# Kernel optimization log

Measured on AMD Instinct MI355X. Metric: run time of the kernel, lower is better.

Reference implementation:

```python
import jax, jax.numpy as jnp
import numpy as np

DIM = 512
HEADS = 8
DIM_HEAD = 64
DIM_INNER = HEADS * DIM_HEAD
SCALE = DIM_HEAD ** -0.5


def setup_inputs() -> dict:
    key = jax.random.key(0)
    ks = jax.random.split(key, 8)
    b, n = 2, 1024
    x = jax.random.normal(ks[0], (b, n, DIM), dtype=jnp.float32)
    w = lambda k, i, o: jax.random.normal(k, (i, o), dtype=jnp.float32) * 0.02
    return {
        'x': x,
        'w_q_u': w(ks[1], DIM, DIM_INNER),
        'w_k_u': w(ks[2], DIM, DIM_INNER),
        'w_v_u': w(ks[3], DIM, DIM_INNER),
        'w_q_c': w(ks[4], DIM, DIM_INNER),
        'w_k_c': w(ks[5], DIM, DIM_INNER),
        'w_v_c': w(ks[6], DIM, DIM_INNER),
        'w_out': w(ks[7], DIM_INNER, DIM),
    }


def reference(x, w_q_u, w_k_u, w_v_u, w_q_c, w_k_c, w_v_c, w_out):
    b, n, _ = x.shape

    def proj(w):  # [b,n,dim] -> [b,h,n,d]
        return (x @ w).reshape(b, n, HEADS, DIM_HEAD).transpose(0, 2, 1, 3)

    q_u, k_u, v_u = proj(w_q_u), proj(w_k_u), proj(w_v_u)
    q_c, k_c, v_c = proj(w_q_c), proj(w_k_c), proj(w_v_c)

    idx = jnp.arange(n)
    causal = idx[:, None] >= idx[None, :]  # tril ones (binary causal mask)

    # term1 = (q_c @ v_u^T) * scale, zeroed above diagonal
    term1 = jnp.einsum('bhid,bhjd->bhij', q_c, v_u) * SCALE
    term1 = term1 * causal.astype(term1.dtype)

    # sigmoid term: (q_u @ k_u^T)*scale with lookahead mask tril(-inf, diag=0)
    logits_u = jnp.einsum('bhid,bhjd->bhij', q_u, k_u) * SCALE
    sig = jax.nn.sigmoid(jnp.where(causal, -jnp.inf, logits_u))

    # S_u[i,k] = sum_j term1[i,j] * sig[k,j]
    S_u = jnp.einsum('bhij,bhkj->bhik', term1, sig)

    # S_c: causal-masked QK
    S_c = jnp.einsum('bhid,bhjd->bhij', q_c, k_c) * SCALE
    S_c = jnp.where(causal, S_c, -jnp.inf)

    final_scores = S_c - jax.nn.silu(S_u)
    attn = jax.nn.softmax(final_scores, axis=-1)
    out = jnp.einsum('bhij,bhjd->bhid', attn, v_c)  # [b,h,n,d]
    out = out.transpose(0, 2, 1, 3).reshape(b, n, DIM_INNER)
    return out @ w_out
```

## Files before the change

### kernel.cpp

```cpp
#include <hip/hip_runtime.h>
#include <math.h>


typedef __bf16 bf16x8 __attribute__((ext_vector_type(8)));
typedef float f32x4 __attribute__((ext_vector_type(4)));

#define SCALE 0.125f

#define GLL(g, l) __builtin_amdgcn_global_load_lds(                         \
    (const __attribute__((address_space(1))) void*)(g),                     \
    (__attribute__((address_space(3))) void*)(l), 16, 0, 0)

__device__ __forceinline__ unsigned short f2bf(float f){
  unsigned int x = __builtin_bit_cast(unsigned int, f);
  unsigned int r = (x + 0x7fffu + ((x >> 16) & 1u)) >> 16;
  return (unsigned short)r;
}
__device__ __forceinline__ float bf2f(unsigned short u){
  unsigned int x = ((unsigned int)u) << 16;
  return __builtin_bit_cast(float, x);
}
__device__ __forceinline__ f32x4 mfma16(bf16x8 a, bf16x8 b, f32x4 c){
  return __builtin_amdgcn_mfma_f32_16x16x32_bf16(a, b, c, 0, 0, 0);
}
__device__ __forceinline__ bf16x8 ld8(const unsigned short* p){
  return *(const bf16x8*)p;
}

__global__ __launch_bounds__(256) void k_prep(
    const float* __restrict__ x,
    const float* __restrict__ w0, const float* __restrict__ w1,
    const float* __restrict__ w2, const float* __restrict__ w3,
    const float* __restrict__ w4, const float* __restrict__ w5,
    const float* __restrict__ w6,
    unsigned short* __restrict__ xb, unsigned short* __restrict__ wT){
  int t = threadIdx.x;
  if (blockIdx.x < 1024){
    int i = blockIdx.x * 256 + t;
    float4 v = ((const float4*)x)[i];
    ushort4 o; o.x = f2bf(v.x); o.y = f2bf(v.y); o.z = f2bf(v.z); o.w = f2bf(v.w);
    ((ushort4*)xb)[i] = o;
    return;
  }
  __shared__ float lds[64 * 65];
  int bx = blockIdx.x - 1024;
  int mat = bx >> 6, tile = bx & 63, tr = tile >> 3, tc = tile & 7;
  int k0 = tr * 64, c0 = tc * 64;
  const float* src;
  switch (mat){
    case 0: src = w0; break; case 1: src = w1; break; case 2: src = w2; break;
    case 3: src = w3; break; case 4: src = w4; break; case 5: src = w5; break;
    default: src = w6; break;
  }
#pragma unroll
  for (int i = 0; i < 4; ++i){
    int r = (t >> 4) + i * 16, c4 = (t & 15) * 4;
    float4 v = *(const float4*)(src + (size_t)(k0 + r) * 512 + c0 + c4);
    lds[r * 65 + c4 + 0] = v.x; lds[r * 65 + c4 + 1] = v.y;
    lds[r * 65 + c4 + 2] = v.z; lds[r * 65 + c4 + 3] = v.w;
  }
  __syncthreads();
  unsigned short* dst = wT + (size_t)mat * 262144;
#pragma unroll
  for (int i = 0; i < 4; ++i){
    int oc = (t >> 4) + i * 16;
    int kq = (t & 15) * 4;
    ushort4 o;
    o.x = f2bf(lds[(kq + 0) * 65 + oc]);
    o.y = f2bf(lds[(kq + 1) * 65 + oc]);
    o.z = f2bf(lds[(kq + 2) * 65 + oc]);
    o.w = f2bf(lds[(kq + 3) * 65 + oc]);
    *(ushort4*)(dst + (size_t)(c0 + oc) * 512 + k0 + kq) = o;
  }
}

__global__ __launch_bounds__(256) void k_proj(
    const unsigned short* __restrict__ xb, const unsigned short* __restrict__ wT,
    unsigned short* __restrict__ P){
  __shared__ unsigned short sA[128 * 32], sB[128 * 32];
  int t = threadIdx.x, lane = t & 63, l16 = lane & 15, quad = lane >> 4;
  int w = t >> 6, wm = w >> 1, wn = w & 1;
  int bx = blockIdx.x;
  int mt = bx / 24, nt = bx - mt * 24;
  int M0 = mt * 128, N0 = nt * 128;
  int matb = N0 >> 9;
  int nin = N0 & 511;
  int srow = (lane >> 2), scol = (lane & 3) * 8;
  const unsigned short* gA = xb + (size_t)(M0 + w*32 + srow) * 512 + scol;
  const unsigned short* gB = wT + (size_t)matb * 262144
                               + (size_t)(nin + w*32 + srow) * 512 + scol;
  unsigned short* lA = sA + (w*32) * 32;
  unsigned short* lB = sB + (w*32) * 32;
  f32x4 acc[4][4] = {};
  for (int k0 = 0; k0 < 512; k0 += 32){
    GLL(gA + k0,            lA);
    GLL(gA + k0 + 16*512,   lA + 16*32);
    GLL(gB + k0,            lB);
    GLL(gB + k0 + 16*512,   lB + 16*32);
    __syncthreads();
    bf16x8 aw[4], ax[4];
#pragma unroll
    for (int fi = 0; fi < 4; ++fi)
      aw[fi] = *(const bf16x8*)(sB + (wn*64 + fi*16 + l16) * 32 + quad * 8);
#pragma unroll
    for (int mi = 0; mi < 4; ++mi)
      ax[mi] = *(const bf16x8*)(sA + (wm*64 + mi*16 + l16) * 32 + quad * 8);
#pragma unroll
    for (int fi = 0; fi < 4; ++fi)
#pragma unroll
      for (int mi = 0; mi < 4; ++mi)
        acc[fi][mi] = mfma16(aw[fi], ax[mi], acc[fi][mi]);
    __syncthreads();
  }
#pragma unroll
  for (int fi = 0; fi < 4; ++fi)
#pragma unroll
    for (int mi = 0; mi < 4; ++mi){
      int row = M0 + wm*64 + mi*16 + l16;
      int b_ = row >> 10, n_ = row & 1023;
      int c0 = N0 + wn*64 + fi*16 + quad*4;
      int h = (c0 & 511) >> 6, d = c0 & 63;
      int bh = b_*8 + h;
      ushort4 o;
      o.x = f2bf(acc[fi][mi][0]); o.y = f2bf(acc[fi][mi][1]);
      o.z = f2bf(acc[fi][mi][2]); o.w = f2bf(acc[fi][mi][3]);
      *(ushort4*)(P + (size_t)(matb*16 + bh) * 65536 + (size_t)n_ * 64 + d) = o;
    }
}

__global__ __launch_bounds__(256) void k_qk_vct(
    const unsigned short* __restrict__ P,
    unsigned short* __restrict__ term1, unsigned short* __restrict__ sig,
    unsigned short* __restrict__ vcT){
  int t = threadIdx.x;
  if (blockIdx.x < 256){
    __shared__ unsigned short lds[64 * 72];
    int bh = blockIdx.x >> 4, nt = blockIdx.x & 15;
    int N0 = nt * 64;
    const unsigned short* src = P + (size_t)(5*16 + bh) * 65536 + (size_t)N0 * 64;
#pragma unroll
    for (int it = 0; it < 2; ++it){
      int id = it * 256 + t;
      int r = id >> 3, c8 = (id & 7) * 8;
      ushort4 v0 = *(const ushort4*)(src + r * 64 + c8);
      ushort4 v1 = *(const ushort4*)(src + r * 64 + c8 + 4);
      *(ushort4*)(lds + r * 72 + c8) = v0;
      *(ushort4*)(lds + r * 72 + c8 + 4) = v1;
    }
    __syncthreads();
    unsigned short* dst = vcT + (size_t)bh * 65536;
#pragma unroll
    for (int it = 0; it < 2; ++it){
      int id = it * 256 + t;
      int dd = id >> 3, n8 = (id & 7) * 8;
      ushort4 a, b;
      a.x = lds[(n8+0)*72 + dd]; a.y = lds[(n8+1)*72 + dd];
      a.z = lds[(n8+2)*72 + dd]; a.w = lds[(n8+3)*72 + dd];
      b.x = lds[(n8+4)*72 + dd]; b.y = lds[(n8+5)*72 + dd];
      b.z = lds[(n8+6)*72 + dd]; b.w = lds[(n8+7)*72 + dd];
      *(ushort4*)(dst + (size_t)dd * 1024 + N0 + n8) = a;
      *(ushort4*)(dst + (size_t)dd * 1024 + N0 + n8 + 4) = b;
    }
    return;
  }
  __shared__ unsigned short sA[128 * 32], sB[128 * 32];
  int id = blockIdx.x - 256;
  int bh = id & 15, tt = id >> 4;
  int mat = (tt >= 36);
  int tl = mat ? tt - 36 : tt;
  int ti = 0;
  while (tl >= ti + 1){ tl -= ti + 1; ++ti; }
  int tj = tl;
  int R0, C0;
  const unsigned short *Asrc, *Bsrc;
  if (!mat){ R0 = ti * 128; C0 = tj * 128;
             Asrc = P + (size_t)(3*16 + bh) * 65536;
             Bsrc = P + (size_t)(2*16 + bh) * 65536; }
  else     { R0 = tj * 128; C0 = ti * 128;
             Asrc = P + (size_t)(0*16 + bh) * 65536;
             Bsrc = P + (size_t)(1*16 + bh) * 65536; }
  int lane = t & 63, l16 = lane & 15, quad = lane >> 4;
  int w = t >> 6, wm = w >> 1, wn = w & 1;
  int srow = lane >> 2, scol = (lane & 3) * 8;
  const unsigned short* gA = Asrc + (size_t)(R0 + w*32 + srow) * 64 + scol;
  const unsigned short* gB = Bsrc + (size_t)(C0 + w*32 + srow) * 64 + scol;
  unsigned short* lA = sA + (w*32) * 32;
  unsigned short* lB = sB + (w*32) * 32;
  f32x4 acc[4][4] = {};
#pragma unroll
  for (int k0 = 0; k0 < 64; k0 += 32){
    GLL(gA + k0,           lA);
    GLL(gA + k0 + 16*64,   lA + 16*32);
    GLL(gB + k0,           lB);
    GLL(gB + k0 + 16*64,   lB + 16*32);
    __syncthreads();
    bf16x8 af[4], bfr[4];
#pragma unroll
    for (int mi = 0; mi < 4; ++mi)
      af[mi] = *(const bf16x8*)(sA + (wm*64 + mi*16 + l16) * 32 + quad * 8);
#pragma unroll
    for (int fi = 0; fi < 4; ++fi)
      bfr[fi] = *(const bf16x8*)(sB + (wn*64 + fi*16 + l16) * 32 + quad * 8);
#pragma unroll
    for (int fi = 0; fi < 4; ++fi)
#pragma unroll
      for (int mi = 0; mi < 4; ++mi)
        acc[fi][mi] = mfma16(bfr[fi], af[mi], acc[fi][mi]);
    __syncthreads();
  }
  unsigned short* out = (mat ? sig : term1) + (size_t)bh * 1048576;
#pragma unroll
  for (int fi = 0; fi < 4; ++fi)
#pragma unroll
    for (int mi = 0; mi < 4; ++mi){
      int row = R0 + wm*64 + mi*16 + l16;
      int c0 = C0 + wn*64 + fi*16 + quad*4;
      ushort4 o;
#pragma unroll
      for (int r = 0; r < 4; ++r){
        int col = c0 + r;
        float v = acc[fi][mi][r] * SCALE;
        unsigned short res;
        if (!mat) res = (col <= row) ? f2bf(v) : (unsigned short)0;
        else      res = (col >  row) ? f2bf(1.f / (1.f + expf(-v))) : (unsigned short)0;
        ((unsigned short*)&o)[r] = res;
      }
      *(ushort4*)(out + (size_t)row * 1024 + c0) = o;
    }
}

__global__ __launch_bounds__(256) void k_scores(
    const unsigned short* __restrict__ P, const unsigned short* __restrict__ term1,
    const unsigned short* __restrict__ sig, unsigned short* __restrict__ finb){
  __shared__ unsigned short sA[128 * 32], sB[128 * 32];
  int t = threadIdx.x;
  int bh = blockIdx.x & 15, tt = blockIdx.x >> 4;
  int k = 1, T = 0;
  while (tt >= T + k){ T += k; ++k; }
  int delta = 8 - k;
  int tj = tt - T, ti = tj + delta;
  int M0 = ti * 128, N0 = tj * 128;
  size_t sbase = (size_t)bh * 1048576;
  int lane = t & 63, l16 = lane & 15, quad = lane >> 4;
  int w = t >> 6, wm = w >> 1, wn = w & 1;
  int srow = (lane >> 2), scol = (lane & 3) * 8;
  unsigned short* lA = sA + (w*32) * 32;
  unsigned short* lB = sB + (w*32) * 32;
  f32x4 acc_u[4][4] = {};
  f32x4 acc_c[4][4] = {};
  {
    const unsigned short* gA = term1 + sbase + (size_t)(M0 + w*32 + srow) * 1024 + scol;
    const unsigned short* gB = sig   + sbase + (size_t)(N0 + w*32 + srow) * 1024 + scol;
    int steps = (delta + 1) * 4;
    for (int s = 0; s < steps; ++s){
      int j0 = N0 + s * 32;
      GLL(gA + j0,             lA);
      GLL(gA + j0 + 16*1024,   lA + 16*32);
      GLL(gB + j0,             lB);
      GLL(gB + j0 + 16*1024,   lB + 16*32);
      __syncthreads();
      bf16x8 af[4], bfr[4];
#pragma unroll
      for (int mi = 0; mi < 4; ++mi)
        af[mi] = *(const bf16x8*)(sA + (wm*64 + mi*16 + l16) * 32 + quad * 8);
#pragma unroll
      for (int fi = 0; fi < 4; ++fi)
        bfr[fi] = *(const bf16x8*)(sB + (wn*64 + fi*16 + l16) * 32 + quad * 8);
#pragma unroll
      for (int fi = 0; fi < 4; ++fi)
#pragma unroll
        for (int mi = 0; mi < 4; ++mi)
          acc_u[fi][mi] = mfma16(bfr[fi], af[mi], acc_u[fi][mi]);
      __syncthreads();
    }
  }
  {
    const unsigned short* Qc = P + (size_t)(3*16 + bh) * 65536;
    const unsigned short* Kc = P + (size_t)(4*16 + bh) * 65536;
#pragma unroll
    for (int k0 = 0; k0 < 64; k0 += 32){
      bf16x8 af[4], bfr[4];
#pragma unroll
      for (int mi = 0; mi < 4; ++mi)
        af[mi] = ld8(Qc + (size_t)(M0 + wm*64 + mi*16 + l16) * 64 + k0 + quad * 8);
#pragma unroll
      for (int fi = 0; fi < 4; ++fi)
        bfr[fi] = ld8(Kc + (size_t)(N0 + wn*64 + fi*16 + l16) * 64 + k0 + quad * 8);
#pragma unroll
      for (int fi = 0; fi < 4; ++fi)
#pragma unroll
        for (int mi = 0; mi < 4; ++mi)
          acc_c[fi][mi] = mfma16(bfr[fi], af[mi], acc_c[fi][mi]);
    }
  }
  unsigned short* out = finb + sbase;
#pragma unroll
  for (int fi = 0; fi < 4; ++fi)
#pragma unroll
    for (int mi = 0; mi < 4; ++mi){
      int row = M0 + wm*64 + mi*16 + l16;
      int c0 = N0 + wn*64 + fi*16 + quad*4;
      ushort4 o;
#pragma unroll
      for (int r = 0; r < 4; ++r){
        float su = acc_u[fi][mi][r];
        float v = acc_c[fi][mi][r] * SCALE - su / (1.f + expf(-su));
        ((unsigned short*)&o)[r] = f2bf(v);
      }
      *(ushort4*)(out + (size_t)row * 1024 + c0) = o;
    }
}

__global__ __launch_bounds__(256) void k_pv_soft(
    const unsigned short* __restrict__ finb, const unsigned short* __restrict__ vcT,
    unsigned short* __restrict__ O){
  __shared__ __align__(16) unsigned char smem[16 * 1032 * 2];
  unsigned short* lp = (unsigned short*)smem;
  float* red = (float*)smem;
  int t = threadIdx.x;
  int bh = blockIdx.x & 15, mt = 63 - (blockIdx.x >> 4);
  int m0 = mt * 16;
  int kceil = ((m0 + 16 + 31) >> 5) << 5;
  {
    int rl = t >> 4, sub = t & 15;
    int rloc = m0 + rl;
    const unsigned short* p = finb + (size_t)bh * 1048576 + (size_t)rloc * 1024;
    float v[8][8];
    float m = -INFINITY;
#pragma unroll
    for (int i = 0; i < 8; ++i){
      int c8 = (sub + 16*i) * 8;
      if (c8 < kceil){
        ushort4 u0 = *(const ushort4*)(p + c8);
        ushort4 u1 = *(const ushort4*)(p + c8 + 4);
        float vv[8] = {bf2f(u0.x), bf2f(u0.y), bf2f(u0.z), bf2f(u0.w),
                       bf2f(u1.x), bf2f(u1.y), bf2f(u1.z), bf2f(u1.w)};
#pragma unroll
        for (int e = 0; e < 8; ++e){
          v[i][e] = (c8 + e <= rloc) ? vv[e] : -INFINITY;
          m = fmaxf(m, v[i][e]);
        }
      }
    }
#pragma unroll
    for (int off = 1; off < 16; off <<= 1) m = fmaxf(m, __shfl_xor(m, off));
    float s = 0.f;
#pragma unroll
    for (int i = 0; i < 8; ++i){
      int c8 = (sub + 16*i) * 8;
      if (c8 < kceil){
#pragma unroll
        for (int e = 0; e < 8; ++e){
          v[i][e] = expf(v[i][e] - m);
          s += v[i][e];
        }
      }
    }
#pragma unroll
    for (int off = 1; off < 16; off <<= 1) s += __shfl_xor(s, off);
    float inv = 1.f / s;
#pragma unroll
    for (int i = 0; i < 8; ++i){
      int c8 = (sub + 16*i) * 8;
      if (c8 < kceil){
        ushort4 o0, o1;
        o0.x = f2bf(v[i][0] * inv); o0.y = f2bf(v[i][1] * inv);
        o0.z = f2bf(v[i][2] * inv); o0.w = f2bf(v[i][3] * inv);
        o1.x = f2bf(v[i][4] * inv); o1.y = f2bf(v[i][5] * inv);
        o1.z = f2bf(v[i][6] * inv); o1.w = f2bf(v[i][7] * inv);
        *(ushort4*)(lp + rl * 1032 + c8) = o0;
        *(ushort4*)(lp + rl * 1032 + c8 + 4) = o1;
      }
    }
  }
  __syncthreads();
  int lane = t & 63, l16 = lane & 15, quad = lane >> 4, w = t >> 6;
  const unsigned short* Bt = vcT + (size_t)bh * 65536;
  int ktot = kceil >> 5;
  int per = (ktot + 3) >> 2;
  int s0 = w * per, s1 = min(s0 + per, ktot);
  f32x4 acc[4] = {};
  for (int s = s0; s < s1; ++s){
    int k0 = s * 32;
    bf16x8 a = *(const bf16x8*)(lp + l16 * 1032 + k0 + quad * 8);
#pragma unroll
    for (int fi = 0; fi < 4; ++fi){
      bf16x8 b = ld8(Bt + (size_t)(fi*16 + l16) * 1024 + k0 + quad * 8);
      acc[fi] = mfma16(a, b, acc[fi]);
    }
  }
  __syncthreads();
#pragma unroll
  for (int fi = 0; fi < 4; ++fi)
#pragma unroll
    for (int r = 0; r < 4; ++r)
      red[w * 1024 + (quad*4 + r) * 64 + fi*16 + l16] = acc[fi][r];
  __syncthreads();
  float4 a0 = ((const float4*)(red + 0*1024))[t];
  float4 a1 = ((const float4*)(red + 1*1024))[t];
  float4 a2 = ((const float4*)(red + 2*1024))[t];
  float4 a3 = ((const float4*)(red + 3*1024))[t];
  ushort4 o;
  o.x = f2bf(a0.x + a1.x + a2.x + a3.x);
  o.y = f2bf(a0.y + a1.y + a2.y + a3.y);
  o.z = f2bf(a0.z + a1.z + a2.z + a3.z);
  o.w = f2bf(a0.w + a1.w + a2.w + a3.w);
  int e = t * 4, row = e >> 6, col = e & 63;
  *(ushort4*)(O + (size_t)bh * 65536 + (size_t)(m0 + row) * 64 + col) = o;
}

__global__ __launch_bounds__(256) void k_out(
    const unsigned short* __restrict__ O, const unsigned short* __restrict__ woT,
    float* __restrict__ out){
  __shared__ float red[4][1024];
  int t = threadIdx.x, lane = t & 63, l16 = lane & 15, quad = lane >> 4, w = t >> 6;
  int mt = blockIdx.x >> 3, nt = blockIdx.x & 7;
  int m0 = mt * 16, n0 = nt * 64;
  int r_ = m0 + l16, b_ = r_ >> 10, n_ = r_ & 1023;
  f32x4 acc[4] = {};
#pragma unroll
  for (int s = 0; s < 4; ++s){
    int kk = w * 128 + s * 32 + quad * 8;
    int h = kk >> 6, dd = kk & 63;
    bf16x8 a = ld8(O + (size_t)(b_*8 + h) * 65536 + (size_t)n_ * 64 + dd);
#pragma unroll
    for (int fi = 0; fi < 4; ++fi){
      bf16x8 b = ld8(woT + (size_t)(n0 + fi*16 + l16) * 512 + kk);
      acc[fi] = mfma16(a, b, acc[fi]);
    }
  }
#pragma unroll
  for (int fi = 0; fi < 4; ++fi)
#pragma unroll
    for (int r = 0; r < 4; ++r)
      red[w][(quad*4 + r) * 64 + fi*16 + l16] = acc[fi][r];
  __syncthreads();
  float4 a0 = ((const float4*)red[0])[t];
  float4 a1 = ((const float4*)red[1])[t];
  float4 a2 = ((const float4*)red[2])[t];
  float4 a3 = ((const float4*)red[3])[t];
  float4 o;
  o.x = a0.x + a1.x + a2.x + a3.x;
  o.y = a0.y + a1.y + a2.y + a3.y;
  o.z = a0.z + a1.z + a2.z + a3.z;
  o.w = a0.w + a1.w + a2.w + a3.w;
  int e = t * 4, row = e >> 6, col = e & 63;
  *(float4*)(out + (size_t)(m0 + row) * 512 + n0 + col) = o;
}

extern "C" void kernel_launch(void* const* d_in, const int* in_sizes, int n_in,
                              void* d_out, int out_size, void* d_ws, size_t ws_size,
                              hipStream_t stream){
  const float* x = (const float*)d_in[0];
  float* out = (float*)d_out;
  unsigned short* ws = (unsigned short*)d_ws;

  unsigned short* wT    = ws;
  unsigned short* xb    = wT    + (size_t)7  * 262144;
  unsigned short* P     = xb    + (size_t)1048576;
  unsigned short* vcT   = P     + (size_t)96 * 65536;
  unsigned short* term1 = vcT   + (size_t)16 * 65536;
  unsigned short* sig   = term1 + (size_t)16 * 1048576;
  unsigned short* O     = sig   + (size_t)16 * 1048576;
  unsigned short* finb  = O     + (size_t)16 * 65536;

  k_prep<<<1472, 256, 0, stream>>>(
      x,
      (const float*)d_in[1], (const float*)d_in[2], (const float*)d_in[3],
      (const float*)d_in[4], (const float*)d_in[5], (const float*)d_in[6],
      (const float*)d_in[7], xb, wT);
  k_proj<<<384, 256, 0, stream>>>(xb, wT, P);
  k_qk_vct<<<1408, 256, 0, stream>>>(P, term1, sig, vcT);
  k_scores<<<576, 256, 0, stream>>>(P, term1, sig, finb);
  k_pv_soft<<<1024, 256, 0, stream>>>(finb, vcT, O);
  k_out<<<1024, 256, 0, stream>>>(O, wT + (size_t)6 * 262144, out);
}
```

Before: 171.8 us.

## Fuse all stages into one persistent cooperative kernel with grid syncs

Replaces the six separate kernel launches with a single cooperative persistent kernel of 512 blocks. Each block loops over the work items of every stage, with grid-wide syncs between stages. The aim is to remove per-launch overhead and the gaps between kernels. In exchange, every block carries the largest shared-memory footprint and the register pressure of all stages, and grid.sync has its own cost. If the cooperative launch fails, the code falls back to the original multi-kernel path.

After: 512.9 us. +198.6%, slower.

```diff
diff --git a/kernel.cpp b/kernel.cpp
--- a/kernel.cpp
+++ b/kernel.cpp
@@ -1,11 +1,15 @@
 #include <hip/hip_runtime.h>
+#include <hip/hip_cooperative_groups.h>
 #include <math.h>
+
+namespace cg = cooperative_groups;
 
 
 typedef __bf16 bf16x8 __attribute__((ext_vector_type(8)));
 typedef float f32x4 __attribute__((ext_vector_type(4)));
 
 #define SCALE 0.125f
+#define GRID 512
 
 #define GLL(g, l) __builtin_amdgcn_global_load_lds(                         \
     (const __attribute__((address_space(1))) void*)(g),                     \
@@ -27,23 +31,21 @@
   return *(const bf16x8*)p;
 }
 
-__global__ __launch_bounds__(256) void k_prep(
-    const float* __restrict__ x,
-    const float* __restrict__ w0, const float* __restrict__ w1,
-    const float* __restrict__ w2, const float* __restrict__ w3,
-    const float* __restrict__ w4, const float* __restrict__ w5,
-    const float* __restrict__ w6,
-    unsigned short* __restrict__ xb, unsigned short* __restrict__ wT){
-  int t = threadIdx.x;
-  if (blockIdx.x < 1024){
-    int i = blockIdx.x * 256 + t;
+
+__device__ __forceinline__ void phase_prep_item(
+    int it, int t, const float* x,
+    const float* w0, const float* w1, const float* w2, const float* w3,
+    const float* w4, const float* w5, const float* w6,
+    unsigned short* xb, unsigned short* wT, unsigned char* smem){
+  if (it < 1024){
+    int i = it * 256 + t;
     float4 v = ((const float4*)x)[i];
     ushort4 o; o.x = f2bf(v.x); o.y = f2bf(v.y); o.z = f2bf(v.z); o.w = f2bf(v.w);
     ((ushort4*)xb)[i] = o;
     return;
   }
-  __shared__ float lds[64 * 65];
-  int bx = blockIdx.x - 1024;
+  float* lds = (float*)smem;
+  int bx = it - 1024;
   int mat = bx >> 6, tile = bx & 63, tr = tile >> 3, tc = tile & 7;
   int k0 = tr * 64, c0 = tc * 64;
   const float* src;
@@ -72,20 +74,21 @@
     o.w = f2bf(lds[(kq + 3) * 65 + oc]);
     *(ushort4*)(dst + (size_t)(c0 + oc) * 512 + k0 + kq) = o;
   }
-}
-
-__global__ __launch_bounds__(256) void k_proj(
-    const unsigned short* __restrict__ xb, const unsigned short* __restrict__ wT,
-    unsigned short* __restrict__ P){
-  __shared__ unsigned short sA[128 * 32], sB[128 * 32];
-  int t = threadIdx.x, lane = t & 63, l16 = lane & 15, quad = lane >> 4;
+  __syncthreads();
+}
+
+__device__ __forceinline__ void phase_proj_item(
+    int it, int t, const unsigned short* xb, const unsigned short* wT,
+    unsigned short* P, unsigned char* smem){
+  unsigned short* sA = (unsigned short*)smem;
+  unsigned short* sB = sA + 128 * 32;
+  int lane = t & 63, l16 = lane & 15, quad = lane >> 4;
   int w = t >> 6, wm = w >> 1, wn = w & 1;
-  int bx = blockIdx.x;
-  int mt = bx / 24, nt = bx - mt * 24;
+  int srow = lane >> 2, scol = (lane & 3) * 8;
+  int mt = it / 24, nt = it - mt * 24;
   int M0 = mt * 128, N0 = nt * 128;
   int matb = N0 >> 9;
   int nin = N0 & 511;
-  int srow = (lane >> 2), scol = (lane & 3) * 8;
   const unsigned short* gA = xb + (size_t)(M0 + w*32 + srow) * 512 + scol;
   const unsigned short* gB = wT + (size_t)matb * 262144
                                + (size_t)(nin + w*32 + srow) * 512 + scol;
@@ -128,19 +131,18 @@
     }
 }
 
-__global__ __launch_bounds__(256) void k_qk_vct(
-    const unsigned short* __restrict__ P,
-    unsigned short* __restrict__ term1, unsigned short* __restrict__ sig,
-    unsigned short* __restrict__ vcT){
-  int t = threadIdx.x;
-  if (blockIdx.x < 256){
-    __shared__ unsigned short lds[64 * 72];
-    int bh = blockIdx.x >> 4, nt = blockIdx.x & 15;
+__device__ __forceinline__ void phase_qkvct_item(
+    int it, int t, const unsigned short* P,
+    unsigned short* term1, unsigned short* sig, unsigned short* vcT,
+    unsigned char* smem){
+  if (it < 256){
+    unsigned short* lds = (unsigned short*)smem;
+    int bh = it >> 4, nt = it & 15;
     int N0 = nt * 64;
     const unsigned short* src = P + (size_t)(5*16 + bh) * 65536 + (size_t)N0 * 64;
 #pragma unroll
-    for (int it = 0; it < 2; ++it){
-      int id = it * 256 + t;
+    for (int i2 = 0; i2 < 2; ++i2){
+      int id = i2 * 256 + t;
       int r = id >> 3, c8 = (id & 7) * 8;
       ushort4 v0 = *(const ushort4*)(src + r * 64 + c8);
       ushort4 v1 = *(const ushort4*)(src + r * 64 + c8 + 4);
@@ -150,8 +152,8 @@
     __syncthreads();
     unsigned short* dst = vcT + (size_t)bh * 65536;
 #pragma unroll
-    for (int it = 0; it < 2; ++it){
-      int id = it * 256 + t;
+    for (int i2 = 0; i2 < 2; ++i2){
+      int id = i2 * 256 + t;
       int dd = id >> 3, n8 = (id & 7) * 8;
       ushort4 a, b;
       a.x = lds[(n8+0)*72 + dd]; a.y = lds[(n8+1)*72 + dd];
@@ -161,10 +163,12 @@
       *(ushort4*)(dst + (size_t)dd * 1024 + N0 + n8) = a;
       *(ushort4*)(dst + (size_t)dd * 1024 + N0 + n8 + 4) = b;
     }
+    __syncthreads();
     return;
   }
-  __shared__ unsigned short sA[128 * 32], sB[128 * 32];
-  int id = blockIdx.x - 256;
+  unsigned short* sA = (unsigned short*)smem;
+  unsigned short* sB = sA + 128 * 32;
+  int id = it - 256;
   int bh = id & 15, tt = id >> 4;
   int mat = (tt >= 36);
   int tl = mat ? tt - 36 : tt;
@@ -208,7 +212,7 @@
         acc[fi][mi] = mfma16(bfr[fi], af[mi], acc[fi][mi]);
     __syncthreads();
   }
-  unsigned short* out = (mat ? sig : term1) + (size_t)bh * 1048576;
+  unsigned short* outp = (mat ? sig : term1) + (size_t)bh * 1048576;
 #pragma unroll
   for (int fi = 0; fi < 4; ++fi)
 #pragma unroll
@@ -225,16 +229,16 @@
         else      res = (col >  row) ? f2bf(1.f / (1.f + expf(-v))) : (unsigned short)0;
         ((unsigned short*)&o)[r] = res;
       }
-      *(ushort4*)(out + (size_t)row * 1024 + c0) = o;
-    }
-}
-
-__global__ __launch_bounds__(256) void k_scores(
-    const unsigned short* __restrict__ P, const unsigned short* __restrict__ term1,
-    const unsigned short* __restrict__ sig, unsigned short* __restrict__ finb){
-  __shared__ unsigned short sA[128 * 32], sB[128 * 32];
-  int t = threadIdx.x;
-  int bh = blockIdx.x & 15, tt = blockIdx.x >> 4;
+      *(ushort4*)(outp + (size_t)row * 1024 + c0) = o;
+    }
+}
+
+__device__ __forceinline__ void phase_scores_item(
+    int it, int t, const unsigned short* P, const unsigned short* term1,
+    const unsigned short* sig, unsigned short* finb, unsigned char* smem){
+  unsigned short* sA = (unsigned short*)smem;
+  unsigned short* sB = sA + 128 * 32;
+  int bh = it & 15, tt = it >> 4;
   int k = 1, T = 0;
   while (tt >= T + k){ T += k; ++k; }
   int delta = 8 - k;
@@ -243,7 +247,7 @@
   size_t sbase = (size_t)bh * 1048576;
   int lane = t & 63, l16 = lane & 15, quad = lane >> 4;
   int w = t >> 6, wm = w >> 1, wn = w & 1;
-  int srow = (lane >> 2), scol = (lane & 3) * 8;
+  int srow = lane >> 2, scol = (lane & 3) * 8;
   unsigned short* lA = sA + (w*32) * 32;
   unsigned short* lB = sB + (w*32) * 32;
   f32x4 acc_u[4][4] = {};
@@ -293,7 +297,7 @@
           acc_c[fi][mi] = mfma16(bfr[fi], af[mi], acc_c[fi][mi]);
     }
   }
-  unsigned short* out = finb + sbase;
+  unsigned short* outp = finb + sbase;
 #pragma unroll
   for (int fi = 0; fi < 4; ++fi)
 #pragma unroll
@@ -307,18 +311,16 @@
         float v = acc_c[fi][mi][r] * SCALE - su / (1.f + expf(-su));
         ((unsigned short*)&o)[r] = f2bf(v);
       }
-      *(ushort4*)(out + (size_t)row * 1024 + c0) = o;
-    }
-}
-
-__global__ __launch_bounds__(256) void k_pv_soft(
-    const unsigned short* __restrict__ finb, const unsigned short* __restrict__ vcT,
-    unsigned short* __restrict__ O){
-  __shared__ __align__(16) unsigned char smem[16 * 1032 * 2];
+      *(ushort4*)(outp + (size_t)row * 1024 + c0) = o;
+    }
+}
+
+__device__ __forceinline__ void phase_pvsoft_item(
+    int it, int t, const unsigned short* finb, const unsigned short* vcT,
+    unsigned short* O, unsigned char* smem){
   unsigned short* lp = (unsigned short*)smem;
   float* red = (float*)smem;
-  int t = threadIdx.x;
-  int bh = blockIdx.x & 15, mt = 63 - (blockIdx.x >> 4);
+  int bh = it & 15, mt = 63 - (it >> 4);
   int m0 = mt * 16;
   int kceil = ((m0 + 16 + 31) >> 5) << 5;
   {
@@ -407,14 +409,15 @@
   o.w = f2bf(a0.w + a1.w + a2.w + a3.w);
   int e = t * 4, row = e >> 6, col = e & 63;
   *(ushort4*)(O + (size_t)bh * 65536 + (size_t)(m0 + row) * 64 + col) = o;
-}
-
-__global__ __launch_bounds__(256) void k_out(
-    const unsigned short* __restrict__ O, const unsigned short* __restrict__ woT,
-    float* __restrict__ out){
-  __shared__ float red[4][1024];
-  int t = threadIdx.x, lane = t & 63, l16 = lane & 15, quad = lane >> 4, w = t >> 6;
-  int mt = blockIdx.x >> 3, nt = blockIdx.x & 7;
+  __syncthreads();
+}
+
+__device__ __forceinline__ void phase_out_item(
+    int it, int t, const unsigned short* O, const unsigned short* woT,
+    float* out, unsigned char* smem){
+  float* red = (float*)smem;
+  int lane = t & 63, l16 = lane & 15, quad = lane >> 4, w = t >> 6;
+  int mt = it >> 3, nt = it & 7;
   int m0 = mt * 16, n0 = nt * 64;
   int r_ = m0 + l16, b_ = r_ >> 10, n_ = r_ & 1023;
   f32x4 acc[4] = {};
@@ -433,12 +436,12 @@
   for (int fi = 0; fi < 4; ++fi)
 #pragma unroll
     for (int r = 0; r < 4; ++r)
-      red[w][(quad*4 + r) * 64 + fi*16 + l16] = acc[fi][r];
-  __syncthreads();
-  float4 a0 = ((const float4*)red[0])[t];
-  float4 a1 = ((const float4*)red[1])[t];
-  float4 a2 = ((const float4*)red[2])[t];
-  float4 a3 = ((const float4*)red[3])[t];
+      red[w * 1024 + (quad*4 + r) * 64 + fi*16 + l16] = acc[fi][r];
+  __syncthreads();
+  float4 a0 = ((const float4*)(red + 0*1024))[t];
+  float4 a1 = ((const float4*)(red + 1*1024))[t];
+  float4 a2 = ((const float4*)(red + 2*1024))[t];
+  float4 a3 = ((const float4*)(red + 3*1024))[t];
   float4 o;
   o.x = a0.x + a1.x + a2.x + a3.x;
   o.y = a0.y + a1.y + a2.y + a3.y;
@@ -446,15 +449,18 @@
   o.w = a0.w + a1.w + a2.w + a3.w;
   int e = t * 4, row = e >> 6, col = e & 63;
   *(float4*)(out + (size_t)(m0 + row) * 512 + n0 + col) = o;
-}
-
-extern "C" void kernel_launch(void* const* d_in, const int* in_sizes, int n_in,
-                              void* d_out, int out_size, void* d_ws, size_t ws_size,
-                              hipStream_t stream){
-  const float* x = (const float*)d_in[0];
-  float* out = (float*)d_out;
-  unsigned short* ws = (unsigned short*)d_ws;
-
+  __syncthreads();
+}
+
+__global__ __launch_bounds__(256, 2) void k_all(
+    const float* __restrict__ x,
+    const float* __restrict__ w0, const float* __restrict__ w1,
+    const float* __restrict__ w2, const float* __restrict__ w3,
+    const float* __restrict__ w4, const float* __restrict__ w5,
+    const float* __restrict__ w6,
+    float* __restrict__ out, unsigned short* __restrict__ ws){
+  cg::grid_group grid = cg::this_grid();
+  __shared__ __align__(16) unsigned char smem[33024];
   unsigned short* wT    = ws;
   unsigned short* xb    = wT    + (size_t)7  * 262144;
   unsigned short* P     = xb    + (size_t)1048576;
@@ -463,15 +469,103 @@
   unsigned short* sig   = term1 + (size_t)16 * 1048576;
   unsigned short* O     = sig   + (size_t)16 * 1048576;
   unsigned short* finb  = O     + (size_t)16 * 65536;
-
-  k_prep<<<1472, 256, 0, stream>>>(
-      x,
-      (const float*)d_in[1], (const float*)d_in[2], (const float*)d_in[3],
-      (const float*)d_in[4], (const float*)d_in[5], (const float*)d_in[6],
-      (const float*)d_in[7], xb, wT);
-  k_proj<<<384, 256, 0, stream>>>(xb, wT, P);
-  k_qk_vct<<<1408, 256, 0, stream>>>(P, term1, sig, vcT);
-  k_scores<<<576, 256, 0, stream>>>(P, term1, sig, finb);
-  k_pv_soft<<<1024, 256, 0, stream>>>(finb, vcT, O);
-  k_out<<<1024, 256, 0, stream>>>(O, wT + (size_t)6 * 262144, out);
-}
+  int t = threadIdx.x;
+
+  for (int it = blockIdx.x; it < 1472; it += GRID)
+    phase_prep_item(it, t, x, w0, w1, w2, w3, w4, w5, w6, xb, wT, smem);
+  grid.sync();
+  for (int it = blockIdx.x; it < 384; it += GRID)
+    phase_proj_item(it, t, xb, wT, P, smem);
+  grid.sync();
+  for (int it = blockIdx.x; it < 1408; it += GRID)
+    phase_qkvct_item(it, t, P, term1, sig, vcT, smem);
+  grid.sync();
+  for (int it = blockIdx.x; it < 576; it += GRID)
+    phase_scores_item(it, t, P, term1, sig, finb, smem);
+  grid.sync();
+  for (int it = blockIdx.x; it < 1024; it += GRID)
+    phase_pvsoft_item(it, t, finb, vcT, O, smem);
+  grid.sync();
+  const unsigned short* woT = wT + (size_t)6 * 262144;
+  for (int it = blockIdx.x; it < 1024; it += GRID)
+    phase_out_item(it, t, O, woT, out, smem);
+}
+
+__global__ __launch_bounds__(256) void k_prep(
+    const float* __restrict__ x,
+    const float* __restrict__ w0, const float* __restrict__ w1,
+    const float* __restrict__ w2, const float* __restrict__ w3,
+    const float* __restrict__ w4, const float* __restrict__ w5,
+    const float* __restrict__ w6,
+    unsigned short* __restrict__ xb, unsigned short* __restrict__ wT){
+  __shared__ __align__(16) unsigned char smem[16640];
+  phase_prep_item(blockIdx.x, threadIdx.x, x, w0, w1, w2, w3, w4, w5, w6,
+                  xb, wT, smem);
+}
+__global__ __launch_bounds__(256) void k_proj(
+    const unsigned short* __restrict__ xb, const unsigned short* __restrict__ wT,
+    unsigned short* __restrict__ P){
+  __shared__ __align__(16) unsigned char smem[16384];
+  phase_proj_item(blockIdx.x, threadIdx.x, xb, wT, P, smem);
+}
+__global__ __launch_bounds__(256) void k_qk_vct(
+    const unsigned short* __restrict__ P,
+    unsigned short* __restrict__ term1, unsigned short* __restrict__ sig,
+    unsigned short* __restrict__ vcT){
+  __shared__ __align__(16) unsigned char smem[16384];
+  phase_qkvct_item(blockIdx.x, threadIdx.x, P, term1, sig, vcT, smem);
+}
+__global__ __launch_bounds__(256) void k_scores(
+    const unsigned short* __restrict__ P, const unsigned short* __restrict__ term1,
+    const unsigned short* __restrict__ sig, unsigned short* __restrict__ finb){
+  __shared__ __align__(16) unsigned char smem[16384];
+  phase_scores_item(blockIdx.x, threadIdx.x, P, term1, sig, finb, smem);
+}
+__global__ __launch_bounds__(256) void k_pv_soft(
+    const unsigned short* __restrict__ finb, const unsigned short* __restrict__ vcT,
+    unsigned short* __restrict__ O){
+  __shared__ __align__(16) unsigned char smem[33024];
+  phase_pvsoft_item(blockIdx.x, threadIdx.x, finb, vcT, O, smem);
+}
+__global__ __launch_bounds__(256) void k_out(
+    const unsigned short* __restrict__ O, const unsigned short* __restrict__ woT,
+    float* __restrict__ out){
+  __shared__ __align__(16) unsigned char smem[16384];
+  phase_out_item(blockIdx.x, threadIdx.x, O, woT, out, smem);
+}
+
+extern "C" void kernel_launch(void* const* d_in, const int* in_sizes, int n_in,
+                              void* d_out, int out_size, void* d_ws, size_t ws_size,
+                              hipStream_t stream){
+  const float* x  = (const float*)d_in[0];
+  const float* w0 = (const float*)d_in[1];
+  const float* w1 = (const float*)d_in[2];
+  const float* w2 = (const float*)d_in[3];
+  const float* w3 = (const float*)d_in[4];
+  const float* w4 = (const float*)d_in[5];
+  const float* w5 = (const float*)d_in[6];
+  const float* w6 = (const float*)d_in[7];
+  float* out = (float*)d_out;
+  unsigned short* ws = (unsigned short*)d_ws;
+
+  void* args[] = {(void*)&x, (void*)&w0, (void*)&w1, (void*)&w2, (void*)&w3,
+                  (void*)&w4, (void*)&w5, (void*)&w6, (void*)&out, (void*)&ws};
+  hipError_t err = hipLaunchCooperativeKernel((const void*)k_all, dim3(GRID),
+                                              dim3(256), args, 0, stream);
+  if (err != hipSuccess){
+    unsigned short* wT    = ws;
+    unsigned short* xb    = wT    + (size_t)7  * 262144;
+    unsigned short* P     = xb    + (size_t)1048576;
+    unsigned short* vcT   = P     + (size_t)96 * 65536;
+    unsigned short* term1 = vcT   + (size_t)16 * 65536;
+    unsigned short* sig   = term1 + (size_t)16 * 1048576;
+    unsigned short* O     = sig   + (size_t)16 * 1048576;
+    unsigned short* finb  = O     + (size_t)16 * 65536;
+    k_prep<<<1472, 256, 0, stream>>>(x, w0, w1, w2, w3, w4, w5, w6, xb, wT);
+    k_proj<<<384, 256, 0, stream>>>(xb, wT, P);
+    k_qk_vct<<<1408, 256, 0, stream>>>(P, term1, sig, vcT);
+    k_scores<<<576, 256, 0, stream>>>(P, term1, sig, finb);
+    k_pv_soft<<<1024, 256, 0, stream>>>(finb, vcT, O);
+    k_out<<<1024, 256, 0, stream>>>(O, wT + (size_t)6 * 262144, out);
+  }
+}
```
